# Optimization experiments

Hardware: AMD Instinct MI355X
Metric: run time of the kernel (lower is better)

Reference implementation:

```python
import jax, jax.numpy as jnp
import numpy as np

B, D, L, K = 4096, 2048, 16384, 64  # batch, input_dim, latent_dim, topk


def setup_inputs() -> dict:
    key = jax.random.key(0)
    k_x, k_w = jax.random.split(key, 2)
    x = jax.random.normal(k_x, (B, D), dtype=jnp.float32)
    # torch init: randn(input_dim, latent_dim) / sqrt(input_dim)
    W_enc = jax.random.normal(k_w, (D, L), dtype=jnp.float32) / np.float32(np.sqrt(D))
    b_enc = jnp.zeros((L,), dtype=jnp.float32)
    b_dec = jnp.zeros((D,), dtype=jnp.float32)
    return {"x": x, "W_enc": W_enc, "b_enc": b_enc, "b_dec": b_dec, "k": K}


def reference(x, W_enc, b_enc, b_dec, k):
    # encode: [B, D] @ [D, L] + [L]
    z = x @ W_enc + b_enc
    # topk sparsify on |z| (do_abs_topk=True): scatter a 0/1 mask, multiply
    _, idx = jax.lax.top_k(jnp.abs(z), k)                      # idx: [B, k]
    rows = jnp.arange(z.shape[0])[:, None]                     # [B, 1]
    mask = jnp.zeros_like(z).at[rows, idx].set(1.0)            # [B, L]
    z_sparse = z * mask
    # decode with tied weights: [B, L] @ [L, D] + [D]
    recon = z_sparse @ W_enc.T + b_dec
    return recon, z_sparse
```

## Files before the change

kernel.cpp:

```cpp
#include <hip/hip_runtime.h>
#include <stdint.h>

#define NB 4096
#define DD 2048
#define LL 16384
#define KT 64
#define WCAP 24
#define TAU 1.2e-2f
#define T3 1e-4f

typedef unsigned short u16;
typedef __bf16 bf16x8 __attribute__((ext_vector_type(8)));
typedef float f32x4 __attribute__((ext_vector_type(4)));
typedef unsigned short u16x4 __attribute__((ext_vector_type(4)));
typedef unsigned short u16x8 __attribute__((ext_vector_type(8)));

__device__ __forceinline__ float bf2f(u16 b) {
  return __uint_as_float(((unsigned)b) << 16);
}
__device__ __forceinline__ u16 f2bf(float f) {
  unsigned u = __float_as_uint(f);
  unsigned r = u + 0x7fffu + ((u >> 16) & 1u);
  return (u16)(r >> 16);
}

__global__ __launch_bounds__(256) void prep_x(const float* __restrict__ X,
                                              u16* __restrict__ Xh) {
  int i = (blockIdx.x * 256 + threadIdx.x) * 4;
  float4 v = *(const float4*)(X + i);
  u16x4 h;
  h[0] = f2bf(v.x); h[1] = f2bf(v.y); h[2] = f2bf(v.z); h[3] = f2bf(v.w);
  *(u16x4*)(Xh + i) = h;
}

__global__ __launch_bounds__(256) void prep_w(const float* __restrict__ W,
                                              u16* __restrict__ Wh,
                                              u16* __restrict__ Wl) {
  __shared__ float tile[64][65];
  int l0 = blockIdx.x * 64, d0 = blockIdx.y * 64;
  int t = threadIdx.x;
  int lx = (t & 15) * 4;
  int dq = t >> 4;
#pragma unroll
  for (int p = 0; p < 4; ++p) {
    int d = dq + p * 16;
    float4 v = *(const float4*)(W + (size_t)(d0 + d) * LL + l0 + lx);
    tile[d][lx + 0] = v.x; tile[d][lx + 1] = v.y;
    tile[d][lx + 2] = v.z; tile[d][lx + 3] = v.w;
  }
  __syncthreads();
  int dx = (t & 15) * 4;
  int lq = t >> 4;
#pragma unroll
  for (int p = 0; p < 4; ++p) {
    int l = lq + p * 16;
    u16x4 h, lo;
#pragma unroll
    for (int q = 0; q < 4; ++q) {
      float w = tile[dx + q][l];
      u16 hb = f2bf(w);
      h[q] = hb;
      lo[q] = f2bf(w - bf2f(hb));
    }
    size_t o = (size_t)(l0 + l) * DD + d0 + dx;
    *(u16x4*)(Wh + o) = h;
    *(u16x4*)(Wl + o) = lo;
  }
}

#define TBM 256
#define TBN 256
#define TBK 64
#define NKT (DD / TBK)

__device__ __forceinline__ void async16(const u16* g, u16* l) {
  __builtin_amdgcn_global_load_lds(
      (const __attribute__((address_space(1))) unsigned int*)g,
      (__attribute__((address_space(3))) unsigned int*)l, 16, 0, 0);
}

#define STAGE(HF, TAU_)                                                      \
  do {                                                                       \
    const u16* g_ = ((HF) < 2 ? Abase : Bbase) +                             \
                    (size_t)(((HF)&1) * 128 + rr) * DD + ((TAU_) << 6) +     \
                    scol;                                                    \
    u16* l_ = ((HF) < 2 ? As : Bs) + ((TAU_)&1) * (TBM * TBK) +              \
              (((HF)&1) * 128) * TBK + t * 8;                                \
    async16(g_, l_);                                                         \
    async16(g_ + (size_t)64 * DD, l_ + 4096);                                \
  } while (0)

#define LDA(DST, DB, MQ)                                                     \
  do {                                                                       \
    const u16* p_ = As + (DB) * (TBM * TBK) + (wm + (MQ)*64 + fr) * TBK;     \
    _Pragma("unroll") for (int i_ = 0; i_ < 4; ++i_) {                       \
      DST[i_][0] = *(const bf16x8*)(p_ + i_ * (16 * TBK) + c0);              \
      DST[i_][1] = *(const bf16x8*)(p_ + i_ * (16 * TBK) + c1);              \
    }                                                                        \
  } while (0)

#define LDBQ(DB, NQ)                                                         \
  do {                                                                       \
    const u16* p_ = Bs + (DB) * (TBN * TBK) + (wn + (NQ)*32 + fr) * TBK;     \
    _Pragma("unroll") for (int j_ = 0; j_ < 2; ++j_) {                       \
      bq[j_][0] = *(const bf16x8*)(p_ + j_ * (16 * TBK) + c0);               \
      bq[j_][1] = *(const bf16x8*)(p_ + j_ * (16 * TBK) + c1);               \
    }                                                                        \
  } while (0)

#define MFMAQ_R(AF, MQ, NQ, IB, IE)                                          \
  do {                                                                       \
    _Pragma("unroll") for (int i_ = (IB); i_ < (IE); ++i_)                   \
        _Pragma("unroll") for (int j_ = 0; j_ < 2; ++j_) {                   \
      f32x4 a_ = acc[(MQ)*4 + i_][(NQ)*2 + j_];                              \
      a_ = __builtin_amdgcn_mfma_f32_16x16x32_bf16(AF[i_][0], bq[j_][0], a_, \
                                                   0, 0, 0);                 \
      a_ = __builtin_amdgcn_mfma_f32_16x16x32_bf16(AF[i_][1], bq[j_][1], a_, \
                                                   0, 0, 0);                 \
      acc[(MQ)*4 + i_][(NQ)*2 + j_] = a_;                                    \
    }                                                                        \
  } while (0)

#define MFMAQ(AF, MQ, NQ) MFMAQ_R(AF, MQ, NQ, 0, 4)

#define BAR __builtin_amdgcn_s_barrier()
#define LGKM0 asm volatile("s_waitcnt lgkmcnt(0)")
#define LGKM8 asm volatile("s_waitcnt lgkmcnt(8)")
#define LGKM12 asm volatile("s_waitcnt lgkmcnt(12)")
#define PRIO1 __builtin_amdgcn_s_setprio(1)
#define PRIO0 __builtin_amdgcn_s_setprio(0)

__global__ __launch_bounds__(512, 2) void encode_gemm(
    const u16* __restrict__ Xh,
    const u16* __restrict__ Wh,
    const float* __restrict__ benc,
    float* __restrict__ Z) {
  __shared__ u16 As[2 * TBM * TBK];
  __shared__ u16 Bs[2 * TBN * TBK];
  int t = threadIdx.x;
  int m0 = blockIdx.y * TBM;
  int n0 = blockIdx.x * TBN;

  int lane = t & 63, w = t >> 6;
  int wm = (w & 1) * 128;
  int wn = (w >> 1) * 64;
  int fr = lane & 15;
  int fq = lane >> 4;
  int c0 = ((fq ^ (fr & 7)) << 3);
  int c1 = (((4 + fq) ^ (fr & 7)) << 3);
  int rr = t >> 3;
  int scol = (((t & 7) ^ (rr & 7)) << 3);

  const u16* Abase = Xh + (size_t)m0 * DD;
  const u16* Bbase = Wh + (size_t)n0 * DD;

  f32x4 acc[8][4] = {};
  bf16x8 af0[4][2], af1[4][2], bq[2][2];

  STAGE(0, 0); STAGE(1, 0); STAGE(2, 0); STAGE(3, 0);
  asm volatile("s_waitcnt vmcnt(4)" ::: "memory");
  STAGE(0, 1); STAGE(1, 1); STAGE(2, 1);
  asm volatile("s_waitcnt vmcnt(6)" ::: "memory");
  BAR;

  for (int it = 0; it < NKT / 2; ++it) {
    const int notlast = (it < NKT / 2 - 1);
    LDBQ(0, 0);
    LDA(af0, 0, 0);
    LDA(af1, 0, 1);
    STAGE(3, 2 * it + 1);
    BAR; LGKM12; PRIO1; MFMAQ_R(af0, 0, 0, 0, 2);
    LGKM8; MFMAQ_R(af0, 0, 0, 2, 4); PRIO0; BAR;
    LGKM0; PRIO1; MFMAQ(af1, 1, 0); PRIO0;
    LDBQ(0, 1);
    BAR;
    if (notlast) STAGE(0, 2 * it + 2);
    BAR; LGKM0; PRIO1; MFMAQ(af0, 0, 1); PRIO0; BAR;
    if (notlast) { STAGE(1, 2 * it + 2); STAGE(2, 2 * it + 2); }
    BAR; PRIO1; MFMAQ(af1, 1, 1); PRIO0;
    if (notlast) asm volatile("s_waitcnt vmcnt(6)" ::: "memory");
    else         asm volatile("s_waitcnt vmcnt(0)" ::: "memory");
    BAR;
    LDBQ(1, 0);
    LDA(af0, 1, 0);
    LDA(af1, 1, 1);
    if (notlast) STAGE(3, 2 * it + 2);
    BAR; LGKM12; PRIO1; MFMAQ_R(af0, 0, 0, 0, 2);
    LGKM8; MFMAQ_R(af0, 0, 0, 2, 4); PRIO0; BAR;
    LGKM0; PRIO1; MFMAQ(af1, 1, 0); PRIO0;
    LDBQ(1, 1);
    BAR;
    if (notlast) STAGE(0, 2 * it + 3);
    BAR; LGKM0; PRIO1; MFMAQ(af0, 0, 1); PRIO0; BAR;
    if (notlast) { STAGE(1, 2 * it + 3); STAGE(2, 2 * it + 3); }
    BAR; PRIO1; MFMAQ(af1, 1, 1); PRIO0;
    if (notlast) asm volatile("s_waitcnt vmcnt(6)" ::: "memory");
    BAR;
  }

  int rbase = m0 + wm + fq * 4;
#pragma unroll
  for (int nr = 0; nr < 4; ++nr) {
    int col = n0 + wn + nr * 16 + fr;
    float be = benc[col];
#pragma unroll
    for (int mr = 0; mr < 8; ++mr) {
      int row = rbase + mr * 16;
#pragma unroll
      for (int r = 0; r < 4; ++r)
        Z[(size_t)(row + r) * LL + col] = acc[mr][nr][r] + be;
    }
  }
}

__global__ __launch_bounds__(512) void topk_kernel(
    const float* __restrict__ Z, float* __restrict__ ZS,
    int* __restrict__ TKI, float* __restrict__ TKV,
    int* __restrict__ WIDX, int* __restrict__ META, int r0) {
  int lrow = blockIdx.x, grow = r0 + lrow, t = threadIdx.x;
  const float* zr = Z + (size_t)lrow * LL;
  float* zs = ZS + (size_t)lrow * LL;

  uint4 kv[8];
#pragma unroll
  for (int i = 0; i < 8; ++i) {
    float4 v = ((const float4*)zr)[t + i * 512];
    kv[i].x = __float_as_uint(v.x) & 0x7fffffffu;
    kv[i].y = __float_as_uint(v.y) & 0x7fffffffu;
    kv[i].z = __float_as_uint(v.z) & 0x7fffffffu;
    kv[i].w = __float_as_uint(v.w) & 0x7fffffffu;
  }
  float4 z4 = {0.f, 0.f, 0.f, 0.f};
#pragma unroll
  for (int i = 0; i < 8; ++i) ((float4*)zs)[t + i * 512] = z4;

  __shared__ int red[2][8];
  unsigned cut = 0;
  for (int bit = 30; bit >= 16; --bit) {
    int ph = bit & 1;
    unsigned ct = cut | (1u << bit);
    int cnt = 0;
#pragma unroll
    for (int i = 0; i < 8; ++i)
      cnt += (kv[i].x >= ct) + (kv[i].y >= ct) + (kv[i].z >= ct) + (kv[i].w >= ct);
    for (int off = 32; off > 0; off >>= 1) cnt += __shfl_down(cnt, off, 64);
    if ((t & 63) == 0) red[ph][t >> 6] = cnt;
    __syncthreads();
    int total = 0;
#pragma unroll
    for (int wv = 0; wv < 8; ++wv) total += red[ph][wv];
    if (total >= KT) cut = ct;
  }

  float c16 = __uint_as_float(cut);
  float cnx = __uint_as_float(cut + 0x10000u);
  float chi = cnx + TAU;
  float clo = c16 - TAU; if (clo < 0.f) clo = 0.f;
  unsigned hiKey = __float_as_uint(chi);
  unsigned loKey = (clo > 0.f) ? __float_as_uint(clo) : 0u;

  __shared__ unsigned nsel, ntie;
  if (t == 0) { nsel = 0; ntie = 0; }
  __syncthreads();

#pragma unroll
  for (int i = 0; i < 8; ++i) {
    int base = 4 * (t + i * 512);
    unsigned k4[4] = {kv[i].x, kv[i].y, kv[i].z, kv[i].w};
#pragma unroll
    for (int q = 0; q < 4; ++q) {
      unsigned key = k4[q];
      int idx = base + q;
      if (key > hiKey) {
        unsigned p = atomicAdd(&nsel, 1u);
        if (p < KT) {
          float v = zr[idx];
          TKI[grow * KT + p] = idx;
          TKV[grow * KT + p] = v;
          zs[idx] = v;
        }
      } else if (key >= loKey) {
        unsigned p = atomicAdd(&ntie, 1u);
        if (p < WCAP) WIDX[grow * WCAP + p] = idx;
      }
    }
  }
  __syncthreads();
  int ns = (int)nsel; if (ns > KT) ns = KT;
  if (t >= ns && t < KT) { TKI[grow * KT + t] = 0; TKV[grow * KT + t] = 0.f; }
  if (t == 0) {
    int wc = (int)ntie; if (wc > WCAP) wc = WCAP;
    META[grow * 2 + 0] = ns;
    META[grow * 2 + 1] = wc;
  }
}

__global__ __launch_bounds__(256) void fixup_kernel(
    const float* __restrict__ X32, const float* __restrict__ W,
    const float* __restrict__ benc, const u16* __restrict__ Wh,
    const u16* __restrict__ Wl, const float* __restrict__ Z,
    float* __restrict__ ZS, const int* __restrict__ WIDX,
    const int* __restrict__ META, int* __restrict__ TKI,
    float* __restrict__ TKV, int r0) {
  int lrow = blockIdx.x, grow = r0 + lrow, t = threadIdx.x;
  int nsure = META[grow * 2 + 0];
  int wcnt = META[grow * 2 + 1];
  int deferred = KT - nsure;
  if (deferred <= 0) return;
  if (deferred > wcnt) deferred = wcnt;

  __shared__ int widx[WCAP];
  if (t < wcnt) widx[t] = WIDX[grow * WCAP + t];
  __syncthreads();

  if (wcnt == deferred) {
    if (t < wcnt) {
      int idx = widx[t];
      float v = Z[(size_t)lrow * LL + idx];
      TKI[grow * KT + nsure + t] = idx;
      TKV[grow * KT + nsure + t] = v;
      ZS[(size_t)lrow * LL + idx] = v;
    }
    return;
  }

  int wid = t >> 6, ln = t & 63;
  __shared__ float xs[DD];
  __shared__ double wz[WCAP];
  __shared__ int exact_flag[WCAP];
  for (int i = t; i < DD; i += 256) xs[i] = X32[(size_t)grow * DD + i];
  __syncthreads();
  for (int j = wid; j < wcnt; j += 4) {
    int idx = widx[j];
    const u16* wh = Wh + (size_t)idx * DD;
    const u16* wl = Wl + (size_t)idx * DD;
    double p = 0.0;
    for (int k = ln; k < DD; k += 64)
      p += (double)xs[k] * ((double)bf2f(wh[k]) + (double)bf2f(wl[k]));
    for (int off = 32; off > 0; off >>= 1) p += __shfl_down(p, off, 64);
    if (ln == 0) wz[j] = p + (double)benc[idx];
  }
  __syncthreads();

  if (t == 0) {
    int taken = 0;
    double b = 0.0;
    for (int s = 0; s < deferred; ++s) {
      int best = -1; double bv = -1.0;
      for (int j = 0; j < wcnt; ++j) {
        if (taken & (1 << j)) continue;
        double a = fabs(wz[j]);
        if (best < 0 || a > bv || (a == bv && widx[j] < widx[best])) { best = j; bv = a; }
      }
      taken |= (1 << best);
      b = bv;
    }
    for (int j = 0; j < wcnt; ++j)
      exact_flag[j] = (fabs(fabs(wz[j]) - b) < (double)T3) ? 1 : 0;
  }
  __syncthreads();
  for (int j = wid; j < wcnt; j += 4) {
    if (!exact_flag[j]) continue;
    int idx = widx[j];
    double p = 0.0;
    for (int k = ln; k < DD; k += 64)
      p += (double)xs[k] * (double)W[(size_t)k * LL + idx];
    for (int off = 32; off > 0; off >>= 1) p += __shfl_down(p, off, 64);
    if (ln == 0) wz[j] = p + (double)benc[idx];
  }
  __syncthreads();

  if (t == 0) {
    int taken = 0;
    for (int s = 0; s < deferred; ++s) {
      int best = -1; double bv = -1.0;
      for (int j = 0; j < wcnt; ++j) {
        if (taken & (1 << j)) continue;
        double a = fabs(wz[j]);
        if (best < 0 || a > bv || (a == bv && widx[j] < widx[best])) { best = j; bv = a; }
      }
      taken |= (1 << best);
      int idx = widx[best];
      float v = (float)wz[best];
      TKI[grow * KT + nsure + s] = idx;
      TKV[grow * KT + nsure + s] = v;
      ZS[(size_t)lrow * LL + idx] = v;
    }
  }
}

__global__ __launch_bounds__(256) void decode_kernel(
    const u16* __restrict__ Wh, const float* __restrict__ bdec,
    const int* __restrict__ TKI, const float* __restrict__ TKV,
    float* __restrict__ OUT) {
  int row = blockIdx.x, t = threadIdx.x;
  __shared__ int sidx[KT];
  __shared__ float sval[KT];
  if (t < KT) {
    sidx[t] = TKI[row * KT + t] & (LL - 1);
    sval[t] = TKV[row * KT + t];
  }
  __syncthreads();
  int d0 = t * 8;
  float acc[8] = {0.f, 0.f, 0.f, 0.f, 0.f, 0.f, 0.f, 0.f};
#pragma unroll 8
  for (int j = 0; j < KT; ++j) {
    const u16x8 wv = *(const u16x8*)(Wh + (size_t)sidx[j] * DD + d0);
    float v = sval[j];
#pragma unroll
    for (int e = 0; e < 8; ++e) acc[e] = fmaf(v, bf2f(wv[e]), acc[e]);
  }
  float4 o0, o1;
  o0.x = acc[0] + bdec[d0 + 0]; o0.y = acc[1] + bdec[d0 + 1];
  o0.z = acc[2] + bdec[d0 + 2]; o0.w = acc[3] + bdec[d0 + 3];
  o1.x = acc[4] + bdec[d0 + 4]; o1.y = acc[5] + bdec[d0 + 5];
  o1.z = acc[6] + bdec[d0 + 6]; o1.w = acc[7] + bdec[d0 + 7];
  float* dst = OUT + (size_t)row * DD + d0;
  *(float4*)dst = o0;
  *(float4*)(dst + 4) = o1;
}

extern "C" void kernel_launch(void* const* d_in, const int* in_sizes, int n_in,
                              void* d_out, int out_size, void* d_ws,
                              size_t ws_size, hipStream_t stream) {
  const float* X = (const float*)d_in[0];
  const float* W = (const float*)d_in[1];
  const float* benc = (const float*)d_in[2];
  const float* bdec = (const float*)d_in[3];

  char* ws = (char*)d_ws;
  const size_t XH_B = (size_t)NB * DD * 2;
  const size_t WH_B = (size_t)LL * DD * 2;
  const size_t TKI_B = (size_t)NB * KT * 4;
  const size_t WIDX_B = (size_t)NB * WCAP * 4;
  const size_t META_B = (size_t)NB * 2 * 4;
  u16* Xh = (u16*)ws;
  u16* Wh = (u16*)(ws + XH_B);
  u16* Wl = (u16*)(ws + XH_B + WH_B);
  int* TKI = (int*)(ws + XH_B + 2 * WH_B);
  float* TKV = (float*)(ws + XH_B + 2 * WH_B + TKI_B);
  int* WIDX = (int*)(ws + XH_B + 2 * WH_B + 2 * TKI_B);
  int* META = (int*)(ws + XH_B + 2 * WH_B + 2 * TKI_B + WIDX_B);
  float* Zc = (float*)(ws + XH_B + 2 * WH_B + 2 * TKI_B + WIDX_B + META_B);

  size_t fixed = XH_B + 2 * WH_B + 2 * TKI_B + WIDX_B + META_B;
  size_t avail = (ws_size > fixed) ? (ws_size - fixed) : 0;
  int chunk = (int)(avail / ((size_t)LL * 4));
  chunk = (chunk / TBM) * TBM;
  if (chunk > NB) chunk = NB;
  if (chunk < TBM) chunk = TBM;

  float* out_recon = (float*)d_out;
  float* out_zs = (float*)d_out + (size_t)NB * DD;

  prep_x<<<NB * DD / 1024, 256, 0, stream>>>(X, Xh);
  prep_w<<<dim3(LL / 64, DD / 64), 256, 0, stream>>>(W, Wh, Wl);
  for (int r0 = 0; r0 < NB; r0 += chunk) {
    int rows = NB - r0; if (rows > chunk) rows = chunk;
    encode_gemm<<<dim3(LL / TBN, rows / TBM), 512, 0, stream>>>(
        Xh + (size_t)r0 * DD, Wh, benc, Zc);
    topk_kernel<<<rows, 512, 0, stream>>>(
        Zc, out_zs + (size_t)r0 * LL, TKI, TKV, WIDX, META, r0);
    fixup_kernel<<<rows, 256, 0, stream>>>(
        X, W, benc, Wh, Wl, Zc, out_zs + (size_t)r0 * LL, WIDX, META, TKI,
        TKV, r0);
  }
  decode_kernel<<<NB, 256, 0, stream>>>(Wh, bdec, TKI, TKV, out_recon);
}
```

Measured before the change: 1.190 ms.

## Trim GEMM barriers, vectorize fixup dot products, cap encode chunk size

The encode GEMM main loop drops several workgroup barriers and merges the three global-to-shared stage loads into one group behind a single barrier, so MFMA runs in longer uninterrupted stretches. The fixup kernel's bf16 hi/lo dot product now uses 4-wide vector loads with a fully unrolled loop, and the exact fp32 recheck loop is unrolled by 4. The row chunk size is capped at 2048, which splits the batch into at least two encode/topk/fixup passes, keeping the Z buffer smaller and more cache-friendly at the cost of extra launches. Removing barriers risks less overlap between waves and possible shared-memory hazards if the remaining waits are not enough.

```diff
diff --git a/kernel.cpp b/kernel.cpp
--- a/kernel.cpp
+++ b/kernel.cpp
@@ -125,8 +125,10 @@
 
 #define BAR __builtin_amdgcn_s_barrier()
 #define LGKM0 asm volatile("s_waitcnt lgkmcnt(0)")
+#define LGKM4 asm volatile("s_waitcnt lgkmcnt(4)")
 #define LGKM8 asm volatile("s_waitcnt lgkmcnt(8)")
 #define LGKM12 asm volatile("s_waitcnt lgkmcnt(12)")
+#define SCHED0 __builtin_amdgcn_sched_barrier(0)
 #define PRIO1 __builtin_amdgcn_s_setprio(1)
 #define PRIO0 __builtin_amdgcn_s_setprio(0)
 
@@ -169,15 +171,13 @@
     LDA(af0, 0, 0);
     LDA(af1, 0, 1);
     STAGE(3, 2 * it + 1);
-    BAR; LGKM12; PRIO1; MFMAQ_R(af0, 0, 0, 0, 2);
-    LGKM8; MFMAQ_R(af0, 0, 0, 2, 4); PRIO0; BAR;
-    LGKM0; PRIO1; MFMAQ(af1, 1, 0); PRIO0;
+    LGKM12; PRIO1; MFMAQ_R(af0, 0, 0, 0, 2);
+    LGKM8;  MFMAQ_R(af0, 0, 0, 2, 4);
+    LGKM0;  MFMAQ(af1, 1, 0); PRIO0;
     LDBQ(0, 1);
-    BAR;
-    if (notlast) STAGE(0, 2 * it + 2);
-    BAR; LGKM0; PRIO1; MFMAQ(af0, 0, 1); PRIO0; BAR;
-    if (notlast) { STAGE(1, 2 * it + 2); STAGE(2, 2 * it + 2); }
-    BAR; PRIO1; MFMAQ(af1, 1, 1); PRIO0;
+    LGKM0; SCHED0; BAR;
+    if (notlast) { STAGE(0, 2 * it + 2); STAGE(1, 2 * it + 2); STAGE(2, 2 * it + 2); }
+    PRIO1; MFMAQ(af0, 0, 1); MFMAQ(af1, 1, 1); PRIO0;
     if (notlast) asm volatile("s_waitcnt vmcnt(6)" ::: "memory");
     else         asm volatile("s_waitcnt vmcnt(0)" ::: "memory");
     BAR;
@@ -185,15 +185,13 @@
     LDA(af0, 1, 0);
     LDA(af1, 1, 1);
     if (notlast) STAGE(3, 2 * it + 2);
-    BAR; LGKM12; PRIO1; MFMAQ_R(af0, 0, 0, 0, 2);
-    LGKM8; MFMAQ_R(af0, 0, 0, 2, 4); PRIO0; BAR;
-    LGKM0; PRIO1; MFMAQ(af1, 1, 0); PRIO0;
+    LGKM12; PRIO1; MFMAQ_R(af0, 0, 0, 0, 2);
+    LGKM8;  MFMAQ_R(af0, 0, 0, 2, 4);
+    LGKM0;  MFMAQ(af1, 1, 0); PRIO0;
     LDBQ(1, 1);
-    BAR;
-    if (notlast) STAGE(0, 2 * it + 3);
-    BAR; LGKM0; PRIO1; MFMAQ(af0, 0, 1); PRIO0; BAR;
-    if (notlast) { STAGE(1, 2 * it + 3); STAGE(2, 2 * it + 3); }
-    BAR; PRIO1; MFMAQ(af1, 1, 1); PRIO0;
+    LGKM0; SCHED0; BAR;
+    if (notlast) { STAGE(0, 2 * it + 3); STAGE(1, 2 * it + 3); STAGE(2, 2 * it + 3); }
+    PRIO1; MFMAQ(af0, 0, 1); MFMAQ(af1, 1, 1); PRIO0;
     if (notlast) asm volatile("s_waitcnt vmcnt(6)" ::: "memory");
     BAR;
   }
@@ -335,8 +333,16 @@
     const u16* wh = Wh + (size_t)idx * DD;
     const u16* wl = Wl + (size_t)idx * DD;
     double p = 0.0;
-    for (int k = ln; k < DD; k += 64)
-      p += (double)xs[k] * ((double)bf2f(wh[k]) + (double)bf2f(wl[k]));
+#pragma unroll
+    for (int kb = 0; kb < 8; ++kb) {
+      int k = kb * 256 + ln * 4;
+      u16x4 h4 = *(const u16x4*)(wh + k);
+      u16x4 l4 = *(const u16x4*)(wl + k);
+      f32x4 x4 = *(const f32x4*)(xs + k);
+#pragma unroll
+      for (int e = 0; e < 4; ++e)
+        p += (double)x4[e] * ((double)bf2f(h4[e]) + (double)bf2f(l4[e]));
+    }
     for (int off = 32; off > 0; off >>= 1) p += __shfl_down(p, off, 64);
     if (ln == 0) wz[j] = p + (double)benc[idx];
   }
@@ -363,6 +369,7 @@
     if (!exact_flag[j]) continue;
     int idx = widx[j];
     double p = 0.0;
+#pragma unroll 4
     for (int k = ln; k < DD; k += 64)
       p += (double)xs[k] * (double)W[(size_t)k * LL + idx];
     for (int off = 32; off > 0; off >>= 1) p += __shfl_down(p, off, 64);
@@ -447,6 +454,7 @@
   size_t avail = (ws_size > fixed) ? (ws_size - fixed) : 0;
   int chunk = (int)(avail / ((size_t)LL * 4));
   chunk = (chunk / TBM) * TBM;
+  if (chunk > 2048) chunk = 2048;
   if (chunk > NB) chunk = NB;
   if (chunk < TBM) chunk = TBM;
 
```

New measurement: 1.177 ms. Within noise of the previous version (-1.1%).
